# Optimization experiments

Measured on AMD Instinct MI355X. Metric: run time of the kernel, lower is better.

Reference implementation:

```python
import jax, jax.numpy as jnp
import numpy as np

N = 20000   # num_nodes
D = 128     # node_dim
H = 128     # hidden_dim (also per-head channels, PyG out_channels is per-head)
EV = 64     # event_dim
NH = 4      # heads
E = 250000  # num edges
NT = 8      # num_event_types
K = 4       # active event types


def setup_inputs() -> dict:
    key = jax.random.key(0)
    ks = jax.random.split(key, 24)
    def w(i, shape, s=0.05):
        return jax.random.normal(ks[i], shape, dtype=jnp.float32) * s
    z = lambda shape: jnp.zeros(shape, jnp.float32)
    o = lambda shape: jnp.ones(shape, jnp.float32)
    return {
        "node_ids": jnp.arange(N, dtype=jnp.int32),
        "event_type_ids": jax.random.randint(ks[0], (K,), 0, NT, dtype=jnp.int32),
        "src": jax.random.randint(ks[1], (E,), 0, N, dtype=jnp.int32),
        "dst": jax.random.randint(ks[2], (E,), 0, N, dtype=jnp.int32),
        "event_features": jax.random.normal(ks[3], (EV,), dtype=jnp.float32),
        "event_intensity": jax.random.uniform(ks[4], (K,), dtype=jnp.float32),
        "node_emb_table": w(5, (N, D), 1.0),
        "event_type_table": w(6, (NT, H), 0.5),
        "ev_w1": w(7, (EV, H)), "ev_b1": z((H,)), "ev_g1": o((H,)), "ev_bt1": z((H,)),
        "ev_w2": w(8, (H, H)), "ev_b2": z((H,)), "ev_g2": o((H,)), "ev_bt2": z((H,)),
        "wq": w(9, (D + H, NH * H)), "bq": z((NH * H,)),
        "wk": w(10, (D + H, NH * H)), "bk": z((NH * H,)),
        "wv": w(11, (D + H, NH * H)), "bv": z((NH * H,)),
        "wskip": w(12, (D + H, H)), "bskip": z((H,)),
        "g0_w": w(13, (H, NH * H)), "g0_as": w(14, (NH, H), 0.1), "g0_ad": w(15, (NH, H), 0.1), "g0_b": z((H,)),
        "g1_w": w(16, (H, NH * H)), "g1_as": w(17, (NH, H), 0.1), "g1_ad": w(18, (NH, H), 0.1), "g1_b": z((H,)),
        "wih": w(19, (H, 4 * H)), "whh": w(20, (H, 4 * H)), "bih": z((4 * H,)), "bhh": z((4 * H,)),
    }


def layer_norm(x, g, b, eps=1e-5):
    mu = jnp.mean(x, axis=-1, keepdims=True)
    var = jnp.mean(jnp.square(x - mu), axis=-1, keepdims=True)
    return (x - mu) * jax.lax.rsqrt(var + eps) * g + b


def segment_softmax(logits, seg, n):
    # logits: [E, NH]; softmax over edges sharing the same destination seg id
    m = jax.ops.segment_max(logits, seg, num_segments=n)
    m = jnp.where(jnp.isfinite(m), m, 0.0)  # guard empty segments
    e = jnp.exp(logits - m[seg])
    s = jax.ops.segment_sum(e, seg, num_segments=n)
    return e / (s[seg] + 1e-16)


def _forward(node_ids, event_type_ids, src, dst,
             event_features, event_intensity, node_emb_table, event_type_table,
             ev_w1, ev_b1, ev_g1, ev_bt1, ev_w2, ev_b2, ev_g2, ev_bt2,
             wq, bq, wk, bk, wv, bv, wskip, bskip,
             g0_w, g0_as, g0_ad, g0_b, g1_w, g1_as, g1_ad, g1_b,
             wih, whh, bih, bhh):
    node_emb = node_emb_table[node_ids]                                      # [N, D]
    # event encoder MLP (dropout off / eval mode)
    e = jax.nn.relu(layer_norm(event_features @ ev_w1 + ev_b1, ev_g1, ev_bt1))
    e = jax.nn.relu(layer_norm(e @ ev_w2 + ev_b2, ev_g2, ev_bt2))            # [H]
    # intensity-weighted mean of active event-type embeddings
    e = e + jnp.mean(event_type_table[event_type_ids] * event_intensity[:, None], axis=0)
    x = jnp.concatenate([node_emb, jnp.broadcast_to(e, (N, H))], axis=1)     # [N, D+H]

    # --- TransformerConv (heads=NH, concat=False -> head mean, root_weight skip) ---
    q = (x @ wq + bq).reshape(N, NH, H)
    k = (x @ wk + bk).reshape(N, NH, H)
    v = (x @ wv + bv).reshape(N, NH, H)
    alpha = jnp.sum(q[dst] * k[src], axis=-1) / jnp.sqrt(jnp.float32(H))     # [E, NH]
    alpha = segment_softmax(alpha, dst, N)
    agg = jax.ops.segment_sum(v[src] * alpha[..., None], dst, num_segments=N)  # [N, NH, H]
    x = agg.mean(axis=1) + x @ wskip + bskip                                 # [N, H]

    sl = jnp.arange(N, dtype=src.dtype)
    src2 = jnp.concatenate([src, sl])
    dst2 = jnp.concatenate([dst, sl])
    for w_, asrc, adst, b_ in ((g0_w, g0_as, g0_ad, g0_b), (g1_w, g1_as, g1_ad, g1_b)):
        xh = (x @ w_).reshape(N, NH, H)
        a_s = jnp.sum(xh * asrc, axis=-1)                                    # [N, NH]
        a_d = jnp.sum(xh * adst, axis=-1)
        ee = jax.nn.leaky_relu(a_s[src2] + a_d[dst2], 0.2)                   # [E+N, NH]
        a = segment_softmax(ee, dst2, N)
        out = jax.ops.segment_sum(xh[src2] * a[..., None], dst2, num_segments=N)
        x = jax.nn.relu(out.mean(axis=1) + b_)                               # [N, H]

    # --- batched LSTMCell, zero initial (h, c); torch gate order i, f, g, o ---
    h0 = jnp.zeros((N, H), x.dtype)
    c0 = jnp.zeros((N, H), x.dtype)
    gates = x @ wih + bih + h0 @ whh + bhh                                   # [N, 4H]
    gi, gf, gg, go = jnp.split(gates, 4, axis=-1)
    c = jax.nn.sigmoid(gf) * c0 + jax.nn.sigmoid(gi) * jnp.tanh(gg)
    h = jax.nn.sigmoid(go) * jnp.tanh(c)
    return h, c


def reference(node_ids, event_type_ids, src, dst,
              event_features, event_intensity, node_emb_table, event_type_table,
              ev_w1, ev_b1, ev_g1, ev_bt1, ev_w2, ev_b2, ev_g2, ev_bt2,
              wq, bq, wk, bk, wv, bv, wskip, bskip,
              g0_w, g0_as, g0_ad, g0_b, g1_w, g1_as, g1_ad, g1_b,
              wih, whh, bih, bhh):
    return _forward(node_ids, event_type_ids, src, dst,
                    event_features, event_intensity, node_emb_table, event_type_table,
                    ev_w1, ev_b1, ev_g1, ev_bt1, ev_w2, ev_b2, ev_g2, ev_bt2,
                    wq, bq, wk, bk, wv, bv, wskip, bskip,
                    g0_w, g0_as, g0_ad, g0_b, g1_w, g1_as, g1_ad, g1_b,
                    wih, whh, bih, bhh)
```

## Files before the change

### kernel.cpp

```cpp
#include <hip/hip_runtime.h>
#include <math.h>

#define D_DIM 128
#define H_DIM 128
#define QKV_N 1664
#define SQRT_H_INV 0.08838834764831845f

typedef unsigned short u16;
typedef unsigned short ushort8v __attribute__((ext_vector_type(8)));
typedef __bf16 bf16x8 __attribute__((ext_vector_type(8)));
typedef float f32x4 __attribute__((ext_vector_type(4)));

__device__ __forceinline__ float grp16_sum(float v) {
  v += __shfl_xor(v, 1);
  v += __shfl_xor(v, 2);
  v += __shfl_xor(v, 4);
  v += __shfl_xor(v, 8);
  return v;
}

__device__ __forceinline__ void split_bf16(float x, u16& h, u16& l) {
  __bf16 hb = (__bf16)x;
  float rm = x - (float)hb;
  __bf16 lb = (__bf16)rm;
  h = __builtin_bit_cast(u16, hb);
  l = __builtin_bit_cast(u16, lb);
}

__global__ __launch_bounds__(128) void k_event(
    const float* __restrict__ ef, int EV,
    const float* __restrict__ w1, const float* __restrict__ b1,
    const float* __restrict__ g1, const float* __restrict__ bt1,
    const float* __restrict__ w2, const float* __restrict__ b2,
    const float* __restrict__ g2, const float* __restrict__ bt2,
    const float* __restrict__ ett, const int* __restrict__ etid,
    const float* __restrict__ inten, int K,
    float* __restrict__ e_out)
{
  __shared__ float sh[H_DIM];
  __shared__ float red[H_DIM];
  const int t = threadIdx.x;

  float acc = b1[t];
  for (int i = 0; i < EV; ++i) acc += ef[i] * w1[i * H_DIM + t];

  red[t] = acc; __syncthreads();
  for (int s = 64; s > 0; s >>= 1) { if (t < s) red[t] += red[t + s]; __syncthreads(); }
  float mu = red[0] / H_DIM; __syncthreads();
  float d = acc - mu;
  red[t] = d * d; __syncthreads();
  for (int s = 64; s > 0; s >>= 1) { if (t < s) red[t] += red[t + s]; __syncthreads(); }
  float var = red[0] / H_DIM; __syncthreads();
  float y = d * rsqrtf(var + 1e-5f) * g1[t] + bt1[t];
  y = fmaxf(y, 0.f);
  sh[t] = y; __syncthreads();

  float acc2 = b2[t];
  for (int i = 0; i < H_DIM; ++i) acc2 += sh[i] * w2[i * H_DIM + t];

  red[t] = acc2; __syncthreads();
  for (int s = 64; s > 0; s >>= 1) { if (t < s) red[t] += red[t + s]; __syncthreads(); }
  mu = red[0] / H_DIM; __syncthreads();
  d = acc2 - mu;
  red[t] = d * d; __syncthreads();
  for (int s = 64; s > 0; s >>= 1) { if (t < s) red[t] += red[t + s]; __syncthreads(); }
  var = red[0] / H_DIM; __syncthreads();
  float y2 = d * rsqrtf(var + 1e-5f) * g2[t] + bt2[t];
  y2 = fmaxf(y2, 0.f);

  float m = 0.f;
  for (int k = 0; k < K; ++k) m += ett[etid[k] * H_DIM + t] * inten[k];
  e_out[t] = y2 + m / (float)K;
}

__global__ __launch_bounds__(256) void k_cvec(
    const float* __restrict__ e,
    const float* __restrict__ wq, const float* __restrict__ bq,
    const float* __restrict__ wk, const float* __restrict__ bk,
    const float* __restrict__ wv, const float* __restrict__ bv,
    const float* __restrict__ wskip, const float* __restrict__ bskip,
    float* __restrict__ cvec)
{
  __shared__ float es[H_DIM];
  const int t = threadIdx.x;
  if (t < H_DIM) es[t] = e[t];
  __syncthreads();
  int j = blockIdx.x * 256 + t;
  if (j >= QKV_N) return;
  const float* W; const float* b; int col; int stride;
  if (j < 512)       { W = wq;    b = bq;    col = j;        stride = 512; }
  else if (j < 1024) { W = wk;    b = bk;    col = j - 512;  stride = 512; }
  else if (j < 1536) { W = wv;    b = bv;    col = j - 1024; stride = 512; }
  else               { W = wskip; b = bskip; col = j - 1536; stride = 128; }
  float a = b[col];
  for (int i = 0; i < H_DIM; ++i) a += es[i] * W[(D_DIM + i) * stride + col];
  cvec[j] = a;
}

__global__ __launch_bounds__(256) void k_pack(
    const float* __restrict__ wq, const float* __restrict__ wk,
    const float* __restrict__ wv, const float* __restrict__ wskip,
    float* __restrict__ B1)
{
  int idx = blockIdx.x * 256 + threadIdx.x;
  if (idx >= D_DIM * QKV_N) return;
  int i = idx / QKV_N, j = idx - i * QKV_N;
  float v;
  if (j < 512)       v = wq[i * 512 + j];
  else if (j < 1024) v = wk[i * 512 + (j - 512)];
  else if (j < 1536) v = wv[i * 512 + (j - 1024)];
  else               v = wskip[i * 128 + (j - 1536)];
  B1[idx] = v;
}

__global__ __launch_bounds__(256) void k_cvec2(
    const float* __restrict__ bih, const float* __restrict__ bhh,
    float* __restrict__ cvec2)
{
  int j = blockIdx.x * 256 + threadIdx.x;
  if (j < 512) cvec2[j] = bih[j] + bhh[j];
}

__global__ __launch_bounds__(256) void k_split_a(
    const float* __restrict__ A, const int* __restrict__ ids,
    u16* __restrict__ hi, u16* __restrict__ lo, int M, int Mpad)
{
  int idx = blockIdx.x * 256 + threadIdx.x;
  if (idx >= Mpad * 16) return;
  int row = idx >> 4, g = idx & 15;
  int gp = g ^ (row & 7);
  size_t dst = (size_t)row * 128 + gp * 8;
  if (row < M) {
    int ar = ids ? ids[row] : row;
    const float* srcp = A + (size_t)ar * 128 + g * 8;
#pragma unroll
    for (int j = 0; j < 8; ++j) {
      u16 h, l;
      split_bf16(srcp[j], h, l);
      hi[dst + j] = h; lo[dst + j] = l;
    }
  } else {
#pragma unroll
    for (int j = 0; j < 8; ++j) { hi[dst + j] = 0; lo[dst + j] = 0; }
  }
}

__global__ __launch_bounds__(256) void k_split_bt(
    const float* __restrict__ W,
    u16* __restrict__ hi, u16* __restrict__ lo, int Nc)
{
  int idx = blockIdx.x * 256 + threadIdx.x;
  if (idx >= Nc * 16) return;
  int n = idx >> 4, g = idx & 15;
  int gp = g ^ (n & 7);
  size_t dst = (size_t)n * 128 + gp * 8;
#pragma unroll
  for (int j = 0; j < 8; ++j) {
    u16 h, l;
    split_bf16(W[(size_t)(g * 8 + j) * Nc + n], h, l);
    hi[dst + j] = h; lo[dst + j] = l;
  }
}

__global__ __launch_bounds__(256, 1) void mfma_gemm(
    const u16* __restrict__ Ahi, const u16* __restrict__ Alo,
    const u16* __restrict__ Bhi, const u16* __restrict__ Blo,
    const float* __restrict__ cvec, float* __restrict__ C, int M, int Nn,
    u16* __restrict__ bf_out, int bf_lo, int bf_hi, int bf_stride, int skipf32)
{
  __shared__ u16 lds[4 * 16384];
  u16* As_hi = lds;
  u16* As_lo = lds + 16384;
  u16* Bs_hi = lds + 32768;
  u16* Bs_lo = lds + 49152;

  const int t = threadIdx.x;
  const int bm = blockIdx.y * 128;
  const int bn = blockIdx.x * 128;

  const u16* gAh = Ahi + (size_t)bm * 128;
  const u16* gAl = Alo + (size_t)bm * 128;
  const u16* gBh = Bhi + (size_t)bn * 128;
  const u16* gBl = Blo + (size_t)bn * 128;

#pragma unroll
  for (int i = 0; i < 8; ++i) {
    int off = (i * 256 + t) * 8;
    *(ushort8v*)&As_hi[off] = *(const ushort8v*)&gAh[off];
    *(ushort8v*)&As_lo[off] = *(const ushort8v*)&gAl[off];
    *(ushort8v*)&Bs_hi[off] = *(const ushort8v*)&gBh[off];
    *(ushort8v*)&Bs_lo[off] = *(const ushort8v*)&gBl[off];
  }
  __syncthreads();

  const int lane = t & 63;
  const int wid = t >> 6;
  const int wr = wid >> 1, wc = wid & 1;
  const int abase = wr * 64 + (lane & 15);
  const int bbase = wc * 64 + (lane & 15);

  f32x4 acc[4][4];
  const f32x4 zero = {0.f, 0.f, 0.f, 0.f};
#pragma unroll
  for (int i = 0; i < 4; ++i)
#pragma unroll
    for (int j = 0; j < 4; ++j) acc[i][j] = zero;

#pragma unroll
  for (int ks = 0; ks < 4; ++ks) {
    const int gp = ((ks << 2) + (lane >> 4)) ^ (lane & 7);
    bf16x8 ah[4], al[4], bh[4], bl[4];
#pragma unroll
    for (int i = 0; i < 4; ++i) {
      int ra = (abase + i * 16) * 128 + gp * 8;
      ah[i] = *(const bf16x8*)&As_hi[ra];
      al[i] = *(const bf16x8*)&As_lo[ra];
      int rb = (bbase + i * 16) * 128 + gp * 8;
      bh[i] = *(const bf16x8*)&Bs_hi[rb];
      bl[i] = *(const bf16x8*)&Bs_lo[rb];
    }
#pragma unroll
    for (int i = 0; i < 4; ++i)
#pragma unroll
      for (int j = 0; j < 4; ++j) {
        acc[i][j] = __builtin_amdgcn_mfma_f32_16x16x32_bf16(ah[i], bh[j], acc[i][j], 0, 0, 0);
        acc[i][j] = __builtin_amdgcn_mfma_f32_16x16x32_bf16(ah[i], bl[j], acc[i][j], 0, 0, 0);
        acc[i][j] = __builtin_amdgcn_mfma_f32_16x16x32_bf16(al[i], bh[j], acc[i][j], 0, 0, 0);
      }
  }

  const int rq = (lane >> 4) << 2;
  const int cq = lane & 15;
#pragma unroll
  for (int j = 0; j < 4; ++j) {
    int col = bn + wc * 64 + j * 16 + cq;
    float cv = cvec ? cvec[col] : 0.f;
    bool inbf = bf_out && col >= bf_lo && col < bf_hi;
    bool wf32 = !(inbf && skipf32);
#pragma unroll
    for (int i = 0; i < 4; ++i) {
#pragma unroll
      for (int r = 0; r < 4; ++r) {
        int row = bm + wr * 64 + i * 16 + rq + r;
        if (row < M) {
          float val = acc[i][j][r] + cv;
          if (wf32) C[(size_t)row * Nn + col] = val;
          if (inbf) bf_out[(size_t)row * bf_stride + (col - bf_lo)] =
              __builtin_bit_cast(u16, (__bf16)val);
        }
      }
    }
  }
}

__global__ __launch_bounds__(256) void k_zero(int* __restrict__ p, int n) {
  int i = blockIdx.x * 256 + threadIdx.x;
  if (i < n) p[i] = 0;
}
__global__ __launch_bounds__(256) void k_count(
    const int* __restrict__ dst, int* __restrict__ counts, int E) {
  int e = blockIdx.x * 256 + threadIdx.x;
  if (e < E) atomicAdd(&counts[dst[e]], 1);
}
__global__ __launch_bounds__(1024) void k_scan(
    const int* __restrict__ counts, int* __restrict__ offs,
    int* __restrict__ cursor, int N)
{
  __shared__ int wsum[16];
  const int t = threadIdx.x;
  const int lane = t & 63;
  const int wid = t >> 6;
  int running = 0;
  for (int base = 0; base < N; base += 1024) {
    int v = (base + t < N) ? counts[base + t] : 0;
    int incl = v;
#pragma unroll
    for (int s = 1; s < 64; s <<= 1) {
      int u = __shfl_up(incl, s);
      if (lane >= s) incl += u;
    }
    if (lane == 63) wsum[wid] = incl;
    __syncthreads();
    if (wid == 0) {
      int w = (lane < 16) ? wsum[lane] : 0;
#pragma unroll
      for (int s = 1; s < 16; s <<= 1) {
        int u = __shfl_up(w, s);
        if (lane >= s) w += u;
      }
      if (lane < 16) wsum[lane] = w;
    }
    __syncthreads();
    int wpre = (wid > 0) ? wsum[wid - 1] : 0;
    int tot = wsum[15];
    int inclg = incl + wpre;
    if (base + t < N) {
      offs[base + t + 1] = running + inclg;
      cursor[base + t] = running + inclg - v;
    }
    running += tot;
    __syncthreads();
  }
  if (t == 0) offs[0] = 0;
}
__global__ __launch_bounds__(256) void k_fill(
    const int* __restrict__ src, const int* __restrict__ dst,
    int* __restrict__ cursor, int* __restrict__ csr_src, int E) {
  int e = blockIdx.x * 256 + threadIdx.x;
  if (e < E) {
    int slot = atomicAdd(&cursor[dst[e]], 1);
    csr_src[slot] = src[e];
  }
}

__global__ __launch_bounds__(256) void k_tconv(
    const float* __restrict__ C1, const u16* __restrict__ KV,
    const int* __restrict__ offs, const int* __restrict__ csr_src,
    u16* __restrict__ Xhi, u16* __restrict__ Xlo, int N)
{
  const int wid = threadIdx.x >> 6;
  const int lane = threadIdx.x & 63;
  const int node = blockIdx.x * 4 + wid;
  if (node >= N) {
    if (lane < 16) {
      size_t dst = (size_t)node * 128 + (size_t)((lane ^ (node & 7)) * 8);
#pragma unroll
      for (int j = 0; j < 8; ++j) { Xhi[dst + j] = 0; Xlo[dst + j] = 0; }
    }
    return;
  }
  const float* crow = C1 + (size_t)node * QKV_N;
  float q[8];
  {
    float4 q0 = *(const float4*)(crow + lane * 8);
    float4 q1 = *(const float4*)(crow + lane * 8 + 4);
    q[0]=q0.x; q[1]=q0.y; q[2]=q0.z; q[3]=q0.w;
    q[4]=q1.x; q[5]=q1.y; q[6]=q1.z; q[7]=q1.w;
  }
  const int beg = offs[node], end = offs[node + 1];
  float mx = -1e30f;
  float ssum = 0.f;
  float acc[8] = {0.f,0.f,0.f,0.f,0.f,0.f,0.f,0.f};

  int e = beg;
  for (; e + 2 <= end; e += 2) {
    int s0 = csr_src[e];
    int s1 = csr_src[e + 1];
    const u16* r0 = KV + (size_t)s0 * 1024 + lane * 8;
    const u16* r1 = KV + (size_t)s1 * 1024 + lane * 8;
    bf16x8 ka = *(const bf16x8*)(r0);
    bf16x8 kb = *(const bf16x8*)(r1);
    bf16x8 va = *(const bf16x8*)(r0 + 512);
    bf16x8 vb = *(const bf16x8*)(r1 + 512);
    float p0 = 0.f, p1 = 0.f;
#pragma unroll
    for (int j = 0; j < 8; ++j) {
      p0 += q[j] * (float)ka[j];
      p1 += q[j] * (float)kb[j];
    }
    p0 = grp16_sum(p0) * SQRT_H_INV;
    p1 = grp16_sum(p1) * SQRT_H_INV;
    float nm = fmaxf(mx, fmaxf(p0, p1));
    float sc = expf(mx - nm);
    float w0 = expf(p0 - nm);
    float w1 = expf(p1 - nm);
    ssum = ssum * sc + w0 + w1;
#pragma unroll
    for (int j = 0; j < 8; ++j)
      acc[j] = acc[j] * sc + w0 * (float)va[j] + w1 * (float)vb[j];
    mx = nm;
  }
  if (e < end) {
    int s0 = csr_src[e];
    const u16* r0 = KV + (size_t)s0 * 1024 + lane * 8;
    bf16x8 ka = *(const bf16x8*)(r0);
    bf16x8 va = *(const bf16x8*)(r0 + 512);
    float p0 = 0.f;
#pragma unroll
    for (int j = 0; j < 8; ++j) p0 += q[j] * (float)ka[j];
    p0 = grp16_sum(p0) * SQRT_H_INV;
    float nm = fmaxf(mx, p0);
    float sc = expf(mx - nm);
    float w0 = expf(p0 - nm);
    ssum = ssum * sc + w0;
#pragma unroll
    for (int j = 0; j < 8; ++j)
      acc[j] = acc[j] * sc + w0 * (float)va[j];
  }

  float inv = 1.f / (ssum + 1e-16f);
#pragma unroll
  for (int j = 0; j < 8; ++j) acc[j] *= inv;
#pragma unroll
  for (int j = 0; j < 8; ++j) {
    acc[j] += __shfl_xor(acc[j], 16);
    acc[j] += __shfl_xor(acc[j], 32);
  }
  if (lane < 16) {
    const float* sk = crow + 1536 + lane * 8;
    size_t dst = (size_t)node * 128 + (size_t)((lane ^ (node & 7)) * 8);
#pragma unroll
    for (int j = 0; j < 8; ++j) {
      float x = 0.25f * acc[j] + sk[j];
      u16 h, l;
      split_bf16(x, h, l);
      Xhi[dst + j] = h; Xlo[dst + j] = l;
    }
  }
}

__global__ __launch_bounds__(256) void k_gat_ad(
    const float* __restrict__ xh, const float* __restrict__ as_w,
    const float* __restrict__ ad_w, float* __restrict__ a_s,
    float* __restrict__ a_d, int N)
{
  const int wid = threadIdx.x >> 6;
  const int lane = threadIdx.x & 63;
  const int node = blockIdx.x * 4 + wid;
  if (node >= N) return;
  const int head = lane >> 4;
  const int c0 = (lane & 15) * 8;
  const float* xr = xh + (size_t)node * 512 + lane * 8;
  float4 x0 = *(const float4*)(xr);
  float4 x1_ = *(const float4*)(xr + 4);
  const float* aw = as_w + head * 128 + c0;
  const float* dw = ad_w + head * 128 + c0;
  float s1 = x0.x*aw[0] + x0.y*aw[1] + x0.z*aw[2] + x0.w*aw[3]
           + x1_.x*aw[4] + x1_.y*aw[5] + x1_.z*aw[6] + x1_.w*aw[7];
  float s2 = x0.x*dw[0] + x0.y*dw[1] + x0.z*dw[2] + x0.w*dw[3]
           + x1_.x*dw[4] + x1_.y*dw[5] + x1_.z*dw[6] + x1_.w*dw[7];
  s1 = grp16_sum(s1);
  s2 = grp16_sum(s2);
  if ((lane & 15) == 0) {
    a_s[node * 4 + head] = s1;
    a_d[node * 4 + head] = s2;
  }
}

__global__ __launch_bounds__(256) void k_gat_agg(
    const float* __restrict__ xh, const u16* __restrict__ xhb,
    const float* __restrict__ a_s, const float* __restrict__ a_d,
    const int* __restrict__ offs, const int* __restrict__ csr_src,
    const float* __restrict__ bias,
    u16* __restrict__ Xhi, u16* __restrict__ Xlo, int N)
{
  const int wid = threadIdx.x >> 6;
  const int lane = threadIdx.x & 63;
  const int node = blockIdx.x * 4 + wid;
  if (node >= N) {
    if (lane < 16) {
      size_t dst = (size_t)node * 128 + (size_t)((lane ^ (node & 7)) * 8);
#pragma unroll
      for (int j = 0; j < 8; ++j) { Xhi[dst + j] = 0; Xlo[dst + j] = 0; }
    }
    return;
  }
  const int head = lane >> 4;
  const float adn = a_d[node * 4 + head];
  const float asn = a_s[node * 4 + head];
  float lself = asn + adn;
  lself = lself >= 0.f ? lself : 0.2f * lself;

  float mx = lself;
  float ssum = 1.f;
  float acc[8];
  {
    const float* xr = xh + (size_t)node * 512 + lane * 8;
    float4 x0 = *(const float4*)(xr);
    float4 x1_ = *(const float4*)(xr + 4);
    acc[0]=x0.x; acc[1]=x0.y; acc[2]=x0.z; acc[3]=x0.w;
    acc[4]=x1_.x; acc[5]=x1_.y; acc[6]=x1_.z; acc[7]=x1_.w;
  }

  const int beg = offs[node], end = offs[node + 1];
  int e = beg;
  for (; e + 2 <= end; e += 2) {
    int s0 = csr_src[e];
    int s1 = csr_src[e + 1];
    float l0 = a_s[s0 * 4 + head] + adn;
    float l1 = a_s[s1 * 4 + head] + adn;
    l0 = l0 >= 0.f ? l0 : 0.2f * l0;
    l1 = l1 >= 0.f ? l1 : 0.2f * l1;
    const u16* r0 = xhb + (size_t)s0 * 512 + lane * 8;
    const u16* r1 = xhb + (size_t)s1 * 512 + lane * 8;
    bf16x8 xa = *(const bf16x8*)(r0);
    bf16x8 xb = *(const bf16x8*)(r1);
    float nm = fmaxf(mx, fmaxf(l0, l1));
    float sc = expf(mx - nm);
    float w0 = expf(l0 - nm);
    float w1 = expf(l1 - nm);
    ssum = ssum * sc + w0 + w1;
#pragma unroll
    for (int j = 0; j < 8; ++j)
      acc[j] = acc[j] * sc + w0 * (float)xa[j] + w1 * (float)xb[j];
    mx = nm;
  }
  if (e < end) {
    int s0 = csr_src[e];
    float l0 = a_s[s0 * 4 + head] + adn;
    l0 = l0 >= 0.f ? l0 : 0.2f * l0;
    const u16* r0 = xhb + (size_t)s0 * 512 + lane * 8;
    bf16x8 xa = *(const bf16x8*)(r0);
    float nm = fmaxf(mx, l0);
    float sc = expf(mx - nm);
    float w0 = expf(l0 - nm);
    ssum = ssum * sc + w0;
#pragma unroll
    for (int j = 0; j < 8; ++j)
      acc[j] = acc[j] * sc + w0 * (float)xa[j];
  }

  float inv = 1.f / (ssum + 1e-16f);
#pragma unroll
  for (int j = 0; j < 8; ++j) acc[j] *= inv;
#pragma unroll
  for (int j = 0; j < 8; ++j) {
    acc[j] += __shfl_xor(acc[j], 16);
    acc[j] += __shfl_xor(acc[j], 32);
  }
  if (lane < 16) {
    const float* b = bias + lane * 8;
    size_t dst = (size_t)node * 128 + (size_t)((lane ^ (node & 7)) * 8);
#pragma unroll
    for (int j = 0; j < 8; ++j) {
      float x = fmaxf(0.25f * acc[j] + b[j], 0.f);
      u16 h, l;
      split_bf16(x, h, l);
      Xhi[dst + j] = h; Xlo[dst + j] = l;
    }
  }
}

__global__ __launch_bounds__(256) void k_lstm(
    const float* __restrict__ gates, float* __restrict__ out, int N)
{
  int idx = blockIdx.x * 256 + threadIdx.x;
  if (idx >= N * 128) return;
  int n = idx >> 7, c = idx & 127;
  const float* g = gates + (size_t)n * 512;
  float gi = g[c], gg = g[256 + c], go = g[384 + c];
  float cv = (1.f / (1.f + expf(-gi))) * tanhf(gg);
  float hv = (1.f / (1.f + expf(-go))) * tanhf(cv);
  out[idx] = hv;
  out[(size_t)N * 128 + idx] = cv;
}

extern "C" void kernel_launch(void* const* d_in, const int* in_sizes, int n_in,
                              void* d_out, int out_size, void* d_ws, size_t ws_size,
                              hipStream_t stream) {
  const int*   node_ids = (const int*)d_in[0];
  const int*   etid     = (const int*)d_in[1];
  const int*   src      = (const int*)d_in[2];
  const int*   dst      = (const int*)d_in[3];
  const float* ef       = (const float*)d_in[4];
  const float* inten    = (const float*)d_in[5];
  const float* nemb     = (const float*)d_in[6];
  const float* ett      = (const float*)d_in[7];
  const float* ev_w1 = (const float*)d_in[8],  *ev_b1 = (const float*)d_in[9];
  const float* ev_g1 = (const float*)d_in[10], *ev_bt1 = (const float*)d_in[11];
  const float* ev_w2 = (const float*)d_in[12], *ev_b2 = (const float*)d_in[13];
  const float* ev_g2 = (const float*)d_in[14], *ev_bt2 = (const float*)d_in[15];
  const float* wq = (const float*)d_in[16], *bq = (const float*)d_in[17];
  const float* wk = (const float*)d_in[18], *bk = (const float*)d_in[19];
  const float* wv = (const float*)d_in[20], *bv = (const float*)d_in[21];
  const float* wskip = (const float*)d_in[22], *bskip = (const float*)d_in[23];
  const float* g0_w = (const float*)d_in[24], *g0_as = (const float*)d_in[25];
  const float* g0_ad = (const float*)d_in[26], *g0_b = (const float*)d_in[27];
  const float* g1_w = (const float*)d_in[28], *g1_as = (const float*)d_in[29];
  const float* g1_ad = (const float*)d_in[30], *g1_b = (const float*)d_in[31];
  const float* wih = (const float*)d_in[32];
  const float* bih = (const float*)d_in[34], *bhh = (const float*)d_in[35];

  const int N = in_sizes[0];
  const int K = in_sizes[1];
  const int E = in_sizes[2];
  const int EV = in_sizes[4];

  const int gridMy = (N + 127) / 128;
  const int Npad = gridMy * 128;

  float* ws = (float*)d_ws;
  size_t o = 0;
  float* e_vec = ws + o; o += 128;
  float* cvec1 = ws + o; o += QKV_N;
  float* cvec2 = ws + o; o += 512;
  float* B1    = ws + o; o += (size_t)128 * QKV_N;
  float* C1    = ws + o; o += (size_t)N * QKV_N;
  float* xh    = ws + o; o += (size_t)N * 512;
  u16* Ahi  = (u16*)(ws + o); o += (size_t)Npad * 64;
  u16* Alo  = (u16*)(ws + o); o += (size_t)Npad * 64;
  u16* XShi = (u16*)(ws + o); o += (size_t)Npad * 64;
  u16* XSlo = (u16*)(ws + o); o += (size_t)Npad * 64;
  u16* Bqhi = (u16*)(ws + o); o += (size_t)QKV_N * 64;
  u16* Bqlo = (u16*)(ws + o); o += (size_t)QKV_N * 64;
  u16* Bg0hi = (u16*)(ws + o); o += 512 * 64;
  u16* Bg0lo = (u16*)(ws + o); o += 512 * 64;
  u16* Bg1hi = (u16*)(ws + o); o += 512 * 64;
  u16* Bg1lo = (u16*)(ws + o); o += 512 * 64;
  u16* Bwhi  = (u16*)(ws + o); o += 512 * 64;
  u16* Bwlo  = (u16*)(ws + o); o += 512 * 64;
  u16* KV   = (u16*)(ws + o); o += (size_t)Npad * 512;
  u16* xhb  = (u16*)(ws + o); o += (size_t)Npad * 256;
  float* a_s   = ws + o; o += (size_t)N * 4;
  float* a_d   = ws + o; o += (size_t)N * 4;
  int* counts  = (int*)(ws + o); o += N;
  int* offs    = (int*)(ws + o); o += (size_t)N + 1;
  int* cursor  = (int*)(ws + o); o += N;
  int* csr_src = (int*)(ws + o); o += E;

  float* out = (float*)d_out;

  const int nodeBlocks = (N + 3) / 4;
  const int nodeBlocksPad = Npad / 4;

  k_event<<<1, 128, 0, stream>>>(ef, EV, ev_w1, ev_b1, ev_g1, ev_bt1,
                                 ev_w2, ev_b2, ev_g2, ev_bt2,
                                 ett, etid, inten, K, e_vec);
  k_cvec<<<(QKV_N + 255) / 256, 256, 0, stream>>>(e_vec, wq, bq, wk, bk, wv, bv,
                                                  wskip, bskip, cvec1);
  k_pack<<<(D_DIM * QKV_N + 255) / 256, 256, 0, stream>>>(wq, wk, wv, wskip, B1);
  k_cvec2<<<2, 256, 0, stream>>>(bih, bhh, cvec2);

  k_split_a<<<(Npad * 16 + 255) / 256, 256, 0, stream>>>(nemb, node_ids, Ahi, Alo, N, Npad);
  k_split_bt<<<(QKV_N * 16 + 255) / 256, 256, 0, stream>>>(B1, Bqhi, Bqlo, QKV_N);
  k_split_bt<<<(512 * 16 + 255) / 256, 256, 0, stream>>>(g0_w, Bg0hi, Bg0lo, 512);
  k_split_bt<<<(512 * 16 + 255) / 256, 256, 0, stream>>>(g1_w, Bg1hi, Bg1lo, 512);
  k_split_bt<<<(512 * 16 + 255) / 256, 256, 0, stream>>>(wih, Bwhi, Bwlo, 512);

  k_zero<<<(N + 255) / 256, 256, 0, stream>>>(counts, N);
  k_count<<<(E + 255) / 256, 256, 0, stream>>>(dst, counts, E);
  k_scan<<<1, 1024, 0, stream>>>(counts, offs, cursor, N);
  k_fill<<<(E + 255) / 256, 256, 0, stream>>>(src, dst, cursor, csr_src, E);

  mfma_gemm<<<dim3(QKV_N / 128, gridMy), 256, 0, stream>>>(
      Ahi, Alo, Bqhi, Bqlo, cvec1, C1, N, QKV_N,
      KV, 512, 1536, 1024, 1);

  k_tconv<<<nodeBlocksPad, 256, 0, stream>>>(C1, KV, offs, csr_src, XShi, XSlo, N);

  mfma_gemm<<<dim3(4, gridMy), 256, 0, stream>>>(
      XShi, XSlo, Bg0hi, Bg0lo, nullptr, xh, N, 512,
      xhb, 0, 512, 512, 0);
  k_gat_ad<<<nodeBlocks, 256, 0, stream>>>(xh, g0_as, g0_ad, a_s, a_d, N);
  k_gat_agg<<<nodeBlocksPad, 256, 0, stream>>>(xh, xhb, a_s, a_d, offs, csr_src,
                                               g0_b, XShi, XSlo, N);

  mfma_gemm<<<dim3(4, gridMy), 256, 0, stream>>>(
      XShi, XSlo, Bg1hi, Bg1lo, nullptr, xh, N, 512,
      xhb, 0, 512, 512, 0);
  k_gat_ad<<<nodeBlocks, 256, 0, stream>>>(xh, g1_as, g1_ad, a_s, a_d, N);
  k_gat_agg<<<nodeBlocksPad, 256, 0, stream>>>(xh, xhb, a_s, a_d, offs, csr_src,
                                               g1_b, XShi, XSlo, N);

  mfma_gemm<<<dim3(4, gridMy), 256, 0, stream>>>(
      XShi, XSlo, Bwhi, Bwlo, cvec2, xh, N, 512,
      nullptr, 0, 0, 0, 0);
  k_lstm<<<((N * 128) + 255) / 256, 256, 0, stream>>>(xh, out, N);
}
```

Baseline: 530.4 us.

## Split GEMM K-loop into two halves with register prefetch and halved LDS

The MFMA GEMM now stages only half of the K=128 dimension in LDS at a time, which halves shared memory to 64 KB and raises the launch bound to two blocks per CU. The second K-half is loaded from global memory into registers while the first half is computed, then written to LDS behind a barrier. The existing XOR swizzle is kept, because swizzled groups stay inside their 8-group half. The aim is to hide global-load latency and gain occupancy, at the cost of extra barriers and more register pressure under the tighter launch bound.

```diff
diff --git a/kernel.cpp b/kernel.cpp
--- a/kernel.cpp
+++ b/kernel.cpp
@@ -162,43 +162,66 @@
   }
 }
 
-__global__ __launch_bounds__(256, 1) void mfma_gemm(
+__global__ __launch_bounds__(256, 2) void mfma_gemm(
     const u16* __restrict__ Ahi, const u16* __restrict__ Alo,
     const u16* __restrict__ Bhi, const u16* __restrict__ Blo,
     const float* __restrict__ cvec, float* __restrict__ C, int M, int Nn,
     u16* __restrict__ bf_out, int bf_lo, int bf_hi, int bf_stride, int skipf32)
 {
-  __shared__ u16 lds[4 * 16384];
+  __shared__ u16 lds[32768];
   u16* As_hi = lds;
-  u16* As_lo = lds + 16384;
-  u16* Bs_hi = lds + 32768;
-  u16* Bs_lo = lds + 49152;
+  u16* As_lo = lds + 8192;
+  u16* Bs_hi = lds + 16384;
+  u16* Bs_lo = lds + 24576;
 
   const int t = threadIdx.x;
   const int bm = blockIdx.y * 128;
   const int bn = blockIdx.x * 128;
-
-  const u16* gAh = Ahi + (size_t)bm * 128;
-  const u16* gAl = Alo + (size_t)bm * 128;
-  const u16* gBh = Bhi + (size_t)bn * 128;
-  const u16* gBl = Blo + (size_t)bn * 128;
-
-#pragma unroll
-  for (int i = 0; i < 8; ++i) {
-    int off = (i * 256 + t) * 8;
-    *(ushort8v*)&As_hi[off] = *(const ushort8v*)&gAh[off];
-    *(ushort8v*)&As_lo[off] = *(const ushort8v*)&gAl[off];
-    *(ushort8v*)&Bs_hi[off] = *(const ushort8v*)&gBh[off];
-    *(ushort8v*)&Bs_lo[off] = *(const ushort8v*)&gBl[off];
-  }
-  __syncthreads();
-
   const int lane = t & 63;
   const int wid = t >> 6;
   const int wr = wid >> 1, wc = wid & 1;
   const int abase = wr * 64 + (lane & 15);
   const int bbase = wc * 64 + (lane & 15);
 
+  int srow[4], sg[4];
+#pragma unroll
+  for (int i = 0; i < 4; ++i) {
+    int idx = i * 256 + t;
+    srow[i] = idx >> 3;
+    sg[i] = idx & 7;
+  }
+
+  ushort8v ra_h[4], ra_l[4], rb_h[4], rb_l[4];
+
+#pragma unroll
+  for (int i = 0; i < 4; ++i) {
+    size_t ga = (size_t)(bm + srow[i]) * 128 + sg[i] * 8;
+    size_t gb = (size_t)(bn + srow[i]) * 128 + sg[i] * 8;
+    ra_h[i] = *(const ushort8v*)&Ahi[ga];
+    ra_l[i] = *(const ushort8v*)&Alo[ga];
+    rb_h[i] = *(const ushort8v*)&Bhi[gb];
+    rb_l[i] = *(const ushort8v*)&Blo[gb];
+  }
+#pragma unroll
+  for (int i = 0; i < 4; ++i) {
+    int lo_ = srow[i] * 64 + sg[i] * 8;
+    *(ushort8v*)&As_hi[lo_] = ra_h[i];
+    *(ushort8v*)&As_lo[lo_] = ra_l[i];
+    *(ushort8v*)&Bs_hi[lo_] = rb_h[i];
+    *(ushort8v*)&Bs_lo[lo_] = rb_l[i];
+  }
+  __syncthreads();
+
+#pragma unroll
+  for (int i = 0; i < 4; ++i) {
+    size_t ga = (size_t)(bm + srow[i]) * 128 + 64 + sg[i] * 8;
+    size_t gb = (size_t)(bn + srow[i]) * 128 + 64 + sg[i] * 8;
+    ra_h[i] = *(const ushort8v*)&Ahi[ga];
+    ra_l[i] = *(const ushort8v*)&Alo[ga];
+    rb_h[i] = *(const ushort8v*)&Bhi[gb];
+    rb_l[i] = *(const ushort8v*)&Blo[gb];
+  }
+
   f32x4 acc[4][4];
   const f32x4 zero = {0.f, 0.f, 0.f, 0.f};
 #pragma unroll
@@ -207,15 +230,49 @@
     for (int j = 0; j < 4; ++j) acc[i][j] = zero;
 
 #pragma unroll
-  for (int ks = 0; ks < 4; ++ks) {
-    const int gp = ((ks << 2) + (lane >> 4)) ^ (lane & 7);
+  for (int ks = 0; ks < 2; ++ks) {
+    const int gl = (((ks & 1) << 2) + (lane >> 4)) ^ (lane & 7);
     bf16x8 ah[4], al[4], bh[4], bl[4];
 #pragma unroll
     for (int i = 0; i < 4; ++i) {
-      int ra = (abase + i * 16) * 128 + gp * 8;
+      int ra = (abase + i * 16) * 64 + gl * 8;
       ah[i] = *(const bf16x8*)&As_hi[ra];
       al[i] = *(const bf16x8*)&As_lo[ra];
-      int rb = (bbase + i * 16) * 128 + gp * 8;
+      int rb = (bbase + i * 16) * 64 + gl * 8;
+      bh[i] = *(const bf16x8*)&Bs_hi[rb];
+      bl[i] = *(const bf16x8*)&Bs_lo[rb];
+    }
+#pragma unroll
+    for (int i = 0; i < 4; ++i)
+#pragma unroll
+      for (int j = 0; j < 4; ++j) {
+        acc[i][j] = __builtin_amdgcn_mfma_f32_16x16x32_bf16(ah[i], bh[j], acc[i][j], 0, 0, 0);
+        acc[i][j] = __builtin_amdgcn_mfma_f32_16x16x32_bf16(ah[i], bl[j], acc[i][j], 0, 0, 0);
+        acc[i][j] = __builtin_amdgcn_mfma_f32_16x16x32_bf16(al[i], bh[j], acc[i][j], 0, 0, 0);
+      }
+  }
+  __syncthreads();
+
+#pragma unroll
+  for (int i = 0; i < 4; ++i) {
+    int lo_ = srow[i] * 64 + sg[i] * 8;
+    *(ushort8v*)&As_hi[lo_] = ra_h[i];
+    *(ushort8v*)&As_lo[lo_] = ra_l[i];
+    *(ushort8v*)&Bs_hi[lo_] = rb_h[i];
+    *(ushort8v*)&Bs_lo[lo_] = rb_l[i];
+  }
+  __syncthreads();
+
+#pragma unroll
+  for (int ks = 2; ks < 4; ++ks) {
+    const int gl = (((ks & 1) << 2) + (lane >> 4)) ^ (lane & 7);
+    bf16x8 ah[4], al[4], bh[4], bl[4];
+#pragma unroll
+    for (int i = 0; i < 4; ++i) {
+      int ra = (abase + i * 16) * 64 + gl * 8;
+      ah[i] = *(const bf16x8*)&As_hi[ra];
+      al[i] = *(const bf16x8*)&As_lo[ra];
+      int rb = (bbase + i * 16) * 64 + gl * 8;
       bh[i] = *(const bf16x8*)&Bs_hi[rb];
       bl[i] = *(const bf16x8*)&Bs_lo[rb];
     }
```

New measurement: 451.0 us. 15.0% less time.
